# Performance work log

Measured on AMD Instinct MI355X. Metric: run time of the kernel, lower is better.

Reference implementation:

```python
import jax, jax.numpy as jnp
import numpy as np

B, N, C_IN, C_OUT = 16, 1024, 256, 256
POOL_RATIO = 0.5  # pooling_ration


def setup_inputs() -> dict:
    key = jax.random.key(0)
    k0, k1, k2, k3 = jax.random.split(key, 4)
    x = jax.random.normal(k0, (B, N, C_IN), dtype=jnp.float32)
    # sparse-ish dense adjacency (as the module stores adj densely)
    adj = (jax.random.uniform(k1, (B, N, N)) < 0.02).astype(jnp.float32)
    mask = jnp.ones((B, N), dtype=jnp.int32)
    n_nodes = jnp.full((B,), N, dtype=jnp.int32)
    stdv = 1.0 / np.sqrt(C_IN)
    W = jax.random.uniform(k2, (C_IN, C_OUT), minval=-stdv, maxval=stdv, dtype=jnp.float32)
    b = jnp.zeros((C_OUT,), dtype=jnp.float32)
    pooling = jax.random.uniform(k3, (C_OUT, 1), minval=-1.0, maxval=1.0, dtype=jnp.float32)
    return {"x": x, "adj": adj, "mask": mask, "n_nodes": n_nodes, "W": W, "b": b, "pooling": pooling}


def reference(x, adj, mask, n_nodes, W, b, pooling):
    # GraphConvolutionLayer: adj @ (x W) + b   (standard Kipf GCN layer)
    h = jnp.einsum('bnm,bmc->bnc', adj, x @ W) + b          # [B,N,C_OUT]
    Bm, Nm, C = h.shape
    # projection score y = (h @ pooling) / ||pooling||
    y = (h.reshape(Bm * Nm, C) @ pooling).reshape(Bm, Nm)
    y = y / jnp.sqrt(jnp.sum(pooling ** 2))
    # ascending sort indices
    idx = jnp.argsort(y, axis=1)                            # [B,N]
    n_remove = (n_nodes.astype(jnp.float32) * (1.0 - POOL_RATIO)).astype(jnp.int32)
    new_n_nodes = n_nodes - n_remove
    # vectorized equivalent of the per-batch loop: among currently-masked nodes
    # (in ascending-score order), zero out the first n_remove[b] of them.
    m_sorted = jnp.take_along_axis(mask, idx, axis=1)       # mask gathered in sorted order
    rank = jnp.cumsum(m_sorted, axis=1) - m_sorted          # exclusive rank among masked
    remove = (m_sorted == 1) & (rank < n_remove[:, None])
    new_sorted = jnp.where(remove, 0, m_sorted)
    inv = jnp.argsort(idx, axis=1)                          # inverse permutation
    new_mask = jnp.take_along_axis(new_sorted, inv, axis=1)  # [B,N] int
    mf = new_mask.astype(h.dtype)
    x_out = h * jnp.tanh(y)[:, :, None] * mf[:, :, None]
    adj_out = mf[:, :, None] * adj * mf[:, None, :]
    return x_out, adj_out, new_mask, new_n_nodes
```

## Files before the change

kernel.cpp:

```cpp
#include <hip/hip_runtime.h>
#include <math.h>

#define Bsz 16
#define Nn  1024

#define ADJ_OFF    (16*1024*256)
#define MASK_OFF   (ADJ_OFF + 16*1024*1024)
#define NN_OFF     (MASK_OFF + 16*1024)

typedef unsigned long long u64;
typedef unsigned short u16;
typedef short bf16x8 __attribute__((ext_vector_type(8)));
typedef float f32x4  __attribute__((ext_vector_type(4)));

static __device__ inline u16 f2bf(float f) {
    unsigned u = __float_as_uint(f);
    u += 0x7fffu + ((u >> 16) & 1u);
    return (u16)(u >> 16);
}

__global__ __launch_bounds__(256) void k1(const float* __restrict__ x,
                                          const float* __restrict__ W,
                                          const float* __restrict__ pool,
                                          u16* __restrict__ XB,
                                          u16* __restrict__ WT,
                                          float* __restrict__ Z) {
    int bid = blockIdx.x, t = threadIdx.x, lane = t & 63, wid = t >> 6;
    if (bid < 256) {
        __shared__ float sp[256];
        __shared__ float swp[256];
        sp[t] = pool[t];
        __syncthreads();
        float acc = 0.f;
        const float* wr = W + t * 256;
        for (int j = 0; j < 256; j += 4) {
            float4 w4 = *(const float4*)&wr[j];
            acc = fmaf(w4.x, sp[j], fmaf(w4.y, sp[j + 1],
                  fmaf(w4.z, sp[j + 2], fmaf(w4.w, sp[j + 3], acc))));
        }
        swp[t] = acc;
        __syncthreads();
        const float* w4p = &swp[lane * 4];
        float wx = w4p[0], wy = w4p[1], wz = w4p[2], ww = w4p[3];
        int base = bid * 64 + wid * 16;
        #pragma unroll 1
        for (int rb = 0; rb < 4; ++rb) {
            float4 v[4];
            #pragma unroll
            for (int k = 0; k < 4; ++k)
                v[k] = ((const float4*)(x + (size_t)(base + rb * 4 + k) * 256))[lane];
            #pragma unroll
            for (int k = 0; k < 4; ++k) {
                int row = base + rb * 4 + k;
                ushort4 o;
                o.x = f2bf(v[k].x); o.y = f2bf(v[k].y); o.z = f2bf(v[k].z); o.w = f2bf(v[k].w);
                ((ushort4*)(XB + (size_t)row * 256))[lane] = o;
                float a = fmaf(v[k].x, wx, fmaf(v[k].y, wy, fmaf(v[k].z, wz, v[k].w * ww)));
                for (int off = 32; off > 0; off >>= 1) a += __shfl_down(a, off, 64);
                if (lane == 0) Z[row] = a;
            }
        }
    } else {
        __shared__ float sT[64][65];
        int bt = bid - 256;
        int tr = (bt >> 2) * 64, tc = (bt & 3) * 64;
        #pragma unroll
        for (int p = 0; p < 4; ++p) {
            int r = p * 16 + (t >> 4), c = (t & 15) * 4;
            float4 w = *(const float4*)&W[(size_t)(tr + r) * 256 + tc + c];
            sT[r][c] = w.x; sT[r][c + 1] = w.y; sT[r][c + 2] = w.z; sT[r][c + 3] = w.w;
        }
        __syncthreads();
        #pragma unroll
        for (int p = 0; p < 2; ++p) {
            int nl = p * 32 + (t >> 3), kl = (t & 7) * 8;
            u16 tmp[8];
            #pragma unroll
            for (int j = 0; j < 8; ++j) tmp[j] = f2bf(sT[kl + j][nl]);
            *(int4*)&WT[(size_t)(tc + nl) * 256 + tr + kl] = *(const int4*)tmp;
        }
    }
}

__global__ __launch_bounds__(256) void k2(const u16* __restrict__ XB,
                                          const u16* __restrict__ WT,
                                          const float* __restrict__ adj,
                                          const float* __restrict__ Z,
                                          u16* __restrict__ XWBT,
                                          u16* __restrict__ AB,
                                          float* __restrict__ Y) {
    int t = threadIdx.x, lane = t & 63, wid = t >> 6;
    if (blockIdx.x < 256) {
        __shared__ short sA[128][72];
        __shared__ short sB[128][72];
        int bm = blockIdx.x >> 1, bn = blockIdx.x & 1;
        int wave = wid;
        int wr = (wave >> 1) * 64, wc = (wave & 1) * 64;
        int fm = lane & 15, fq = lane >> 4;

        f32x4 acc[4][4];
        #pragma unroll
        for (int i = 0; i < 4; ++i)
            #pragma unroll
            for (int j = 0; j < 4; ++j)
                acc[i][j] = (f32x4){0.f, 0.f, 0.f, 0.f};

        int sr = t >> 1, half = (t & 1) * 32;
        const u16* gA = XB + ((size_t)(bm * 128 + sr)) * 256 + half;
        const u16* gB = WT + ((size_t)(bn * 128 + sr)) * 256 + half;

        for (int kt = 0; kt < 4; ++kt) {
            __syncthreads();
            #pragma unroll
            for (int q = 0; q < 4; ++q) {
                *(int4*)&sA[sr][half + q * 8] = *(const int4*)&gA[kt * 64 + q * 8];
                *(int4*)&sB[sr][half + q * 8] = *(const int4*)&gB[kt * 64 + q * 8];
            }
            __syncthreads();
            #pragma unroll
            for (int ks = 0; ks < 64; ks += 32) {
                bf16x8 af[4], bfv[4];
                #pragma unroll
                for (int i = 0; i < 4; ++i)
                    af[i] = *(const bf16x8*)&sA[wr + i * 16 + fm][ks + fq * 8];
                #pragma unroll
                for (int j = 0; j < 4; ++j)
                    bfv[j] = *(const bf16x8*)&sB[wc + j * 16 + fm][ks + fq * 8];
                #pragma unroll
                for (int i = 0; i < 4; ++i)
                    #pragma unroll
                    for (int j = 0; j < 4; ++j)
                        acc[i][j] = __builtin_amdgcn_mfma_f32_16x16x32_bf16(af[i], bfv[j], acc[i][j], 0, 0, 0);
            }
        }
        int b = bm >> 3;
        #pragma unroll
        for (int i = 0; i < 4; ++i) {
            int rloc = (bm & 7) * 128 + wr + i * 16 + fq * 4;
            #pragma unroll
            for (int j = 0; j < 4; ++j) {
                int c = bn * 128 + wc + j * 16 + fm;
                u16 tmp[4];
                #pragma unroll
                for (int r = 0; r < 4; ++r) tmp[r] = f2bf(acc[i][j][r]);
                *(unsigned long long*)&XWBT[(size_t)b * 262144 + (size_t)c * 1024 + rloc] =
                    *(const unsigned long long*)tmp;
            }
        }
    } else {
        int g = blockIdx.x - 256;
        int b = g >> 6, grp = g & 63;
        __shared__ float sZ[1024];
        ((float4*)sZ)[t] = ((const float4*)(Z + (b << 10)))[t];
        __syncthreads();
        const float* z0 = &sZ[lane * 4];
        #pragma unroll 1
        for (int rr = 0; rr < 4; ++rr) {
            int row = (b << 10) + grp * 16 + wid * 4 + rr;
            const float4* ar = (const float4*)(adj + (size_t)row * 1024);
            float4 v0 = ar[lane], v1 = ar[64 + lane], v2 = ar[128 + lane], v3 = ar[192 + lane];
            u16* abr = AB + (size_t)row * 1024;
            ushort4 o0, o1, o2, o3;
            o0.x = f2bf(v0.x); o0.y = f2bf(v0.y); o0.z = f2bf(v0.z); o0.w = f2bf(v0.w);
            o1.x = f2bf(v1.x); o1.y = f2bf(v1.y); o1.z = f2bf(v1.z); o1.w = f2bf(v1.w);
            o2.x = f2bf(v2.x); o2.y = f2bf(v2.y); o2.z = f2bf(v2.z); o2.w = f2bf(v2.w);
            o3.x = f2bf(v3.x); o3.y = f2bf(v3.y); o3.z = f2bf(v3.z); o3.w = f2bf(v3.w);
            ((ushort4*)abr)[lane] = o0;
            ((ushort4*)abr)[64 + lane] = o1;
            ((ushort4*)abr)[128 + lane] = o2;
            ((ushort4*)abr)[192 + lane] = o3;
            float a = v0.x * z0[0] + v0.y * z0[1] + v0.z * z0[2] + v0.w * z0[3];
            a += v1.x * z0[256] + v1.y * z0[257] + v1.z * z0[258] + v1.w * z0[259];
            a += v2.x * z0[512] + v2.y * z0[513] + v2.z * z0[514] + v2.w * z0[515];
            a += v3.x * z0[768] + v3.y * z0[769] + v3.z * z0[770] + v3.w * z0[771];
            for (int off = 32; off > 0; off >>= 1) a += __shfl_down(a, off, 64);
            if (lane == 0) Y[row] = a;
        }
    }
}

__device__ inline u64 shfl_xor_u64(u64 v, int m) {
    int lo = __shfl_xor((int)(v & 0xffffffffULL), m, 64);
    int hi = __shfl_xor((int)(v >> 32), m, 64);
    return ((u64)(unsigned)hi << 32) | (unsigned)lo;
}

__global__ __launch_bounds__(1024) void k3(const float* __restrict__ Y,
                                           const int* __restrict__ maskIn,
                                           const int* __restrict__ nNodes,
                                           const float* __restrict__ bias,
                                           const float* __restrict__ pool,
                                           float* __restrict__ SCALE,
                                           float* __restrict__ NM,
                                           float* __restrict__ newN,
                                           u64* __restrict__ NMBITS) {
    __shared__ u64 s[1024];
    __shared__ int wsum[16];
    __shared__ int nmLoc[1024];
    __shared__ float redb[4], redq[4];
    __shared__ float sBP, sINV;

    int b = blockIdx.x, t = threadIdx.x, lane = t & 63, wid = t >> 6;
    int base = b << 10;

    if (t < 256) {
        float pv = pool[t];
        float bv = bias[t] * pv;
        float qv = pv * pv;
        for (int off = 32; off > 0; off >>= 1) {
            bv += __shfl_down(bv, off, 64);
            qv += __shfl_down(qv, off, 64);
        }
        if (lane == 0) { redb[wid] = bv; redq[wid] = qv; }
    }
    __syncthreads();
    if (t == 0) {
        sBP  = redb[0] + redb[1] + redb[2] + redb[3];
        sINV = 1.0f / sqrtf(redq[0] + redq[1] + redq[2] + redq[3]);
    }

    float ky = Y[base + t];
    unsigned u = __float_as_uint(ky);
    u = (u & 0x80000000u) ? ~u : (u | 0x80000000u);
    u64 val = ((u64)u << 32) | (unsigned)t;

    for (int k = 2; k <= 1024; k <<= 1) {
        bool up = ((t & k) == 0);
        int j = k >> 1;
        for (; j >= 64; j >>= 1) {
            s[t] = val; __syncthreads();
            u64 p = s[t ^ j]; __syncthreads();
            bool keepMin = (up == ((t & j) == 0));
            bool pLess = p < val;
            val = (keepMin == pLess) ? p : val;
        }
        for (; j >= 1; j >>= 1) {
            u64 p = shfl_xor_u64(val, j);
            bool keepMin = (up == ((t & j) == 0));
            bool pLess = p < val;
            val = (keepMin == pLess) ? p : val;
        }
    }

    int idx = (int)(val & 1023u);
    int mval = maskIn[base + idx];
    int sc = mval;
    for (int off = 1; off < 64; off <<= 1) {
        int nv = __shfl_up(sc, off, 64);
        if (lane >= off) sc += nv;
    }
    if (lane == 63) wsum[wid] = sc;
    __syncthreads();
    int offset = 0;
    for (int w = 0; w < wid; ++w) offset += wsum[w];
    int rank = sc + offset - mval;
    int nn = nNodes[b];
    int nrem = (int)((float)nn * 0.5f);
    int nm = (mval == 1 && rank < nrem) ? 0 : mval;
    nmLoc[idx] = nm;
    NM[base + idx] = (float)nm;
    if (t == 0) newN[b] = (float)(nn - nrem);
    __syncthreads();

    int myNm = nmLoc[t];
    u64 bmask = __ballot(myNm != 0);
    if (lane == 0) NMBITS[b * 16 + wid] = bmask;
    float yr = Y[base + t];
    SCALE[base + t] = myNm ? tanhf((yr + sBP) * sINV) : 0.0f;
}

__global__ __launch_bounds__(256) void k4(const u16* __restrict__ AB,
                                          const u16* __restrict__ XWBT,
                                          const float* __restrict__ SCALE,
                                          const float* __restrict__ bias,
                                          const u64* __restrict__ NMBITS,
                                          float* __restrict__ XO,
                                          float* __restrict__ AO) {
    int t = threadIdx.x, lane = t & 63, wid = t >> 6;
    if (blockIdx.x < 256) {
        __shared__ short sA[128][72];
        __shared__ short sB[128][72];
        int idx = blockIdx.x;
        int bn = idx & 1, bmt = (idx >> 1) & 7, b = idx >> 4;
        int wr = (wid >> 1) * 64, wc = (wid & 1) * 64;
        int fm = lane & 15, fq = lane >> 4;

        f32x4 acc[4][4];
        #pragma unroll
        for (int i = 0; i < 4; ++i)
            #pragma unroll
            for (int j = 0; j < 4; ++j)
                acc[i][j] = (f32x4){0.f, 0.f, 0.f, 0.f};

        int sr = t >> 1, half = (t & 1) * 32;
        const u16* gA = AB + ((size_t)(b * 1024 + bmt * 128 + sr)) * 1024 + half;
        const u16* gB = XWBT + (size_t)b * 262144 + (size_t)(bn * 128 + sr) * 1024 + half;

        for (int kt = 0; kt < 16; ++kt) {
            __syncthreads();
            #pragma unroll
            for (int q = 0; q < 4; ++q) {
                *(int4*)&sA[sr][half + q * 8] = *(const int4*)&gA[kt * 64 + q * 8];
                *(int4*)&sB[sr][half + q * 8] = *(const int4*)&gB[kt * 64 + q * 8];
            }
            __syncthreads();
            #pragma unroll
            for (int ks = 0; ks < 64; ks += 32) {
                bf16x8 af[4], bfv[4];
                #pragma unroll
                for (int i = 0; i < 4; ++i)
                    af[i] = *(const bf16x8*)&sA[wr + i * 16 + fm][ks + fq * 8];
                #pragma unroll
                for (int j = 0; j < 4; ++j)
                    bfv[j] = *(const bf16x8*)&sB[wc + j * 16 + fm][ks + fq * 8];
                #pragma unroll
                for (int i = 0; i < 4; ++i)
                    #pragma unroll
                    for (int j = 0; j < 4; ++j)
                        acc[i][j] = __builtin_amdgcn_mfma_f32_16x16x32_bf16(af[i], bfv[j], acc[i][j], 0, 0, 0);
            }
        }
        float bj[4];
        #pragma unroll
        for (int j = 0; j < 4; ++j) bj[j] = bias[bn * 128 + wc + j * 16 + fm];
        int mb = (b << 10) + bmt * 128 + wr;
        #pragma unroll
        for (int i = 0; i < 4; ++i) {
            int m0 = mb + i * 16 + fq * 4;
            float s0 = SCALE[m0], s1 = SCALE[m0 + 1], s2 = SCALE[m0 + 2], s3 = SCALE[m0 + 3];
            #pragma unroll
            for (int j = 0; j < 4; ++j) {
                int c = bn * 128 + wc + j * 16 + fm;
                float* xo = XO + (size_t)m0 * 256 + c;
                xo[0]   = (acc[i][j][0] + bj[j]) * s0;
                xo[256] = (acc[i][j][1] + bj[j]) * s1;
                xo[512] = (acc[i][j][2] + bj[j]) * s2;
                xo[768] = (acc[i][j][3] + bj[j]) * s3;
            }
        }
    } else {
        int g = blockIdx.x - 256;
        int b = g >> 6, grp = g & 63;
        __shared__ u64 sBits[16];
        if (t < 16) sBits[t] = NMBITS[b * 16 + t];
        __syncthreads();
        int c0 = t * 4;
        u64 wb = sBits[c0 >> 6] >> (c0 & 63);
        float m0 = (wb & 1) ? 1.f : 0.f;
        float m1 = ((wb >> 1) & 1) ? 1.f : 0.f;
        float m2 = ((wb >> 2) & 1) ? 1.f : 0.f;
        float m3 = ((wb >> 3) & 1) ? 1.f : 0.f;
        #pragma unroll 1
        for (int r = 0; r < 16; ++r) {
            int rloc = grp * 16 + r;
            int nmRow = (int)((sBits[rloc >> 6] >> (rloc & 63)) & 1ULL);
            float4* aor = (float4*)(AO + (size_t)((b << 10) + rloc) * 1024);
            if (nmRow) {
                ushort4 ab = ((const ushort4*)(AB + (size_t)((b << 10) + rloc) * 1024))[t];
                float4 o;
                o.x = ab.x ? m0 : 0.f;
                o.y = ab.y ? m1 : 0.f;
                o.z = ab.z ? m2 : 0.f;
                o.w = ab.w ? m3 : 0.f;
                aor[t] = o;
            } else {
                aor[t] = make_float4(0.f, 0.f, 0.f, 0.f);
            }
        }
    }
}

extern "C" void kernel_launch(void* const* d_in, const int* in_sizes, int n_in,
                              void* d_out, int out_size, void* d_ws, size_t ws_size,
                              hipStream_t stream) {
    const float* x      = (const float*)d_in[0];
    const float* adj    = (const float*)d_in[1];
    const int*   mask   = (const int*)d_in[2];
    const int*   nnodes = (const int*)d_in[3];
    const float* W      = (const float*)d_in[4];
    const float* bias   = (const float*)d_in[5];
    const float* pool   = (const float*)d_in[6];

    float* out = (float*)d_out;
    float* XO  = out;
    float* AO  = out + ADJ_OFF;
    float* NM  = out + MASK_OFF;
    float* NNo = out + NN_OFF;

    char* w = (char*)d_ws;
    u16*   XB     = (u16*)(w);
    u16*   WT     = (u16*)(w + 8388608);
    u16*   XWBT   = (u16*)(w + 8519680);
    u16*   AB     = (u16*)(w + 16908288);
    float* Z      = (float*)(w + 50462720);
    float* Y      = (float*)(w + 50528256);
    float* SCALE  = (float*)(w + 50593792);
    u64*   NMBITS = (u64*)(w + 50659328);

    k1<<<272, 256, 0, stream>>>(x, W, pool, XB, WT, Z);
    k2<<<1280, 256, 0, stream>>>(XB, WT, adj, Z, XWBT, AB, Y);
    k3<<<Bsz, 1024, 0, stream>>>(Y, mask, nnodes, bias, pool, SCALE, NM, NNo, NMBITS);
    k4<<<1280, 256, 0, stream>>>(AB, XWBT, SCALE, bias, NMBITS, XO, AO);
}
```

Before: 207.0 us.

## Fuse adjacency masking into GEMM, drop bf16 adj buffer, rank-count sort

k2 no longer writes a bf16 copy of the adjacency. k4 now reads fp32 adj directly, converts it to bf16 into shared memory for the MFMA GEMM and writes the masked adj_out from the same load. This removes a full write and re-read of a 32MB intermediate. k3 replaces the single-block-per-batch bitonic sort with a per-element O(N) rank count spread over 4 blocks per batch. The cost is more shared-memory comparison work in k3 and a smaller GEMM tile (32x256) in k4, which reloads the B operand 32 times per batch.

```diff
diff --git a/kernel.cpp b/kernel.cpp
--- a/kernel.cpp
+++ b/kernel.cpp
@@ -87,15 +87,13 @@
                                           const float* __restrict__ adj,
                                           const float* __restrict__ Z,
                                           u16* __restrict__ XWBT,
-                                          u16* __restrict__ AB,
                                           float* __restrict__ Y) {
     int t = threadIdx.x, lane = t & 63, wid = t >> 6;
     if (blockIdx.x < 256) {
         __shared__ short sA[128][72];
         __shared__ short sB[128][72];
         int bm = blockIdx.x >> 1, bn = blockIdx.x & 1;
-        int wave = wid;
-        int wr = (wave >> 1) * 64, wc = (wave & 1) * 64;
+        int wr = (wid >> 1) * 64, wc = (wid & 1) * 64;
         int fm = lane & 15, fq = lane >> 4;
 
         f32x4 acc[4][4];
@@ -159,16 +157,6 @@
             int row = (b << 10) + grp * 16 + wid * 4 + rr;
             const float4* ar = (const float4*)(adj + (size_t)row * 1024);
             float4 v0 = ar[lane], v1 = ar[64 + lane], v2 = ar[128 + lane], v3 = ar[192 + lane];
-            u16* abr = AB + (size_t)row * 1024;
-            ushort4 o0, o1, o2, o3;
-            o0.x = f2bf(v0.x); o0.y = f2bf(v0.y); o0.z = f2bf(v0.z); o0.w = f2bf(v0.w);
-            o1.x = f2bf(v1.x); o1.y = f2bf(v1.y); o1.z = f2bf(v1.z); o1.w = f2bf(v1.w);
-            o2.x = f2bf(v2.x); o2.y = f2bf(v2.y); o2.z = f2bf(v2.z); o2.w = f2bf(v2.w);
-            o3.x = f2bf(v3.x); o3.y = f2bf(v3.y); o3.z = f2bf(v3.z); o3.w = f2bf(v3.w);
-            ((ushort4*)abr)[lane] = o0;
-            ((ushort4*)abr)[64 + lane] = o1;
-            ((ushort4*)abr)[128 + lane] = o2;
-            ((ushort4*)abr)[192 + lane] = o3;
             float a = v0.x * z0[0] + v0.y * z0[1] + v0.z * z0[2] + v0.w * z0[3];
             a += v1.x * z0[256] + v1.y * z0[257] + v1.z * z0[258] + v1.w * z0[259];
             a += v2.x * z0[512] + v2.y * z0[513] + v2.z * z0[514] + v2.w * z0[515];
@@ -179,31 +167,28 @@
     }
 }
 
-__device__ inline u64 shfl_xor_u64(u64 v, int m) {
-    int lo = __shfl_xor((int)(v & 0xffffffffULL), m, 64);
-    int hi = __shfl_xor((int)(v >> 32), m, 64);
-    return ((u64)(unsigned)hi << 32) | (unsigned)lo;
-}
-
-__global__ __launch_bounds__(1024) void k3(const float* __restrict__ Y,
-                                           const int* __restrict__ maskIn,
-                                           const int* __restrict__ nNodes,
-                                           const float* __restrict__ bias,
-                                           const float* __restrict__ pool,
-                                           float* __restrict__ SCALE,
-                                           float* __restrict__ NM,
-                                           float* __restrict__ newN,
-                                           u64* __restrict__ NMBITS) {
-    __shared__ u64 s[1024];
-    __shared__ int wsum[16];
-    __shared__ int nmLoc[1024];
+__global__ __launch_bounds__(256) void k3(const float* __restrict__ Y,
+                                          const int* __restrict__ maskIn,
+                                          const int* __restrict__ nNodes,
+                                          const float* __restrict__ bias,
+                                          const float* __restrict__ pool,
+                                          float* __restrict__ SCALE,
+                                          float* __restrict__ NM,
+                                          float* __restrict__ newN,
+                                          u64* __restrict__ NMBITS) {
+    __shared__ float sy[1024];
+    __shared__ int   sm[1024];
     __shared__ float redb[4], redq[4];
     __shared__ float sBP, sINV;
-
-    int b = blockIdx.x, t = threadIdx.x, lane = t & 63, wid = t >> 6;
+    int b = blockIdx.x >> 2, part = blockIdx.x & 3;
+    int t = threadIdx.x, lane = t & 63, wid = t >> 6;
     int base = b << 10;
 
-    if (t < 256) {
+    for (int j = t; j < 1024; j += 256) {
+        sy[j] = Y[base + j];
+        sm[j] = maskIn[base + j];
+    }
+    {
         float pv = pool[t];
         float bv = bias[t] * pv;
         float qv = pv * pv;
@@ -218,154 +203,127 @@
         sBP  = redb[0] + redb[1] + redb[2] + redb[3];
         sINV = 1.0f / sqrtf(redq[0] + redq[1] + redq[2] + redq[3]);
     }
-
-    float ky = Y[base + t];
-    unsigned u = __float_as_uint(ky);
-    u = (u & 0x80000000u) ? ~u : (u | 0x80000000u);
-    u64 val = ((u64)u << 32) | (unsigned)t;
-
-    for (int k = 2; k <= 1024; k <<= 1) {
-        bool up = ((t & k) == 0);
-        int j = k >> 1;
-        for (; j >= 64; j >>= 1) {
-            s[t] = val; __syncthreads();
-            u64 p = s[t ^ j]; __syncthreads();
-            bool keepMin = (up == ((t & j) == 0));
-            bool pLess = p < val;
-            val = (keepMin == pLess) ? p : val;
-        }
-        for (; j >= 1; j >>= 1) {
-            u64 p = shfl_xor_u64(val, j);
-            bool keepMin = (up == ((t & j) == 0));
-            bool pLess = p < val;
-            val = (keepMin == pLess) ? p : val;
-        }
-    }
-
-    int idx = (int)(val & 1023u);
-    int mval = maskIn[base + idx];
-    int sc = mval;
-    for (int off = 1; off < 64; off <<= 1) {
-        int nv = __shfl_up(sc, off, 64);
-        if (lane >= off) sc += nv;
-    }
-    if (lane == 63) wsum[wid] = sc;
     __syncthreads();
-    int offset = 0;
-    for (int w = 0; w < wid; ++w) offset += wsum[w];
-    int rank = sc + offset - mval;
+
+    int i = part * 256 + t;
+    float yi = sy[i];
+    int cnt = 0;
+    #pragma unroll 4
+    for (int j = 0; j < 1024; ++j) {
+        float yj = sy[j];
+        bool less = (yj < yi) || (yj == yi && j < i);
+        cnt += less ? sm[j] : 0;
+    }
     int nn = nNodes[b];
     int nrem = (int)((float)nn * 0.5f);
-    int nm = (mval == 1 && rank < nrem) ? 0 : mval;
-    nmLoc[idx] = nm;
-    NM[base + idx] = (float)nm;
-    if (t == 0) newN[b] = (float)(nn - nrem);
-    __syncthreads();
-
-    int myNm = nmLoc[t];
-    u64 bmask = __ballot(myNm != 0);
-    if (lane == 0) NMBITS[b * 16 + wid] = bmask;
-    float yr = Y[base + t];
-    SCALE[base + t] = myNm ? tanhf((yr + sBP) * sINV) : 0.0f;
-}
-
-__global__ __launch_bounds__(256) void k4(const u16* __restrict__ AB,
+    int mi = sm[i];
+    int nm = (mi == 1 && cnt < nrem) ? 0 : mi;
+    NM[base + i] = (float)nm;
+    SCALE[base + i] = nm ? tanhf((yi + sBP) * sINV) : 0.0f;
+    u64 bm = __ballot(nm != 0);
+    if (lane == 0) NMBITS[b * 16 + part * 4 + wid] = bm;
+    if (t == 0 && part == 0) newN[b] = (float)(nn - nrem);
+}
+
+__global__ __launch_bounds__(256) void k4(const float* __restrict__ adj,
                                           const u16* __restrict__ XWBT,
                                           const float* __restrict__ SCALE,
                                           const float* __restrict__ bias,
                                           const u64* __restrict__ NMBITS,
                                           float* __restrict__ XO,
                                           float* __restrict__ AO) {
+    __shared__ short sA[32][72];
+    __shared__ short sB[256][72];
+    __shared__ u64 sBits[16];
     int t = threadIdx.x, lane = t & 63, wid = t >> 6;
-    if (blockIdx.x < 256) {
-        __shared__ short sA[128][72];
-        __shared__ short sB[128][72];
-        int idx = blockIdx.x;
-        int bn = idx & 1, bmt = (idx >> 1) & 7, b = idx >> 4;
-        int wr = (wid >> 1) * 64, wc = (wid & 1) * 64;
-        int fm = lane & 15, fq = lane >> 4;
-
-        f32x4 acc[4][4];
-        #pragma unroll
-        for (int i = 0; i < 4; ++i)
+    int b = blockIdx.x >> 5, mt = blockIdx.x & 31;
+    int m0 = mt * 32;
+    if (t < 16) sBits[t] = NMBITS[b * 16 + t];
+
+    int wc = wid * 64;
+    int fm = lane & 15, fq = lane >> 4;
+
+    f32x4 acc[2][4];
+    #pragma unroll
+    for (int i = 0; i < 2; ++i)
+        #pragma unroll
+        for (int j = 0; j < 4; ++j)
+            acc[i][j] = (f32x4){0.f, 0.f, 0.f, 0.f};
+
+    int ar = t >> 3, c8 = (t & 7) * 8;
+    const float* adjR = adj + ((size_t)((b << 10) + m0 + ar)) * 1024 + c8;
+    float*       aoR  = AO  + ((size_t)((b << 10) + m0 + ar)) * 1024 + c8;
+    const u16*   xwB  = XWBT + (size_t)b * 262144;
+
+    __syncthreads();
+    int rloc = m0 + ar;
+    float rowM = (float)((sBits[rloc >> 6] >> (rloc & 63)) & 1ULL);
+
+    for (int kt = 0; kt < 16; ++kt) {
+        int k0 = kt * 64;
+        __syncthreads();
+        {
+            float4 v0 = *(const float4*)&adjR[k0];
+            float4 v1 = *(const float4*)&adjR[k0 + 4];
+            unsigned cb = (unsigned)((sBits[(k0 + c8) >> 6] >> ((k0 + c8) & 63)) & 0xffULL);
+            float4 o0, o1;
+            o0.x = (cb & 1u)   ? v0.x * rowM : 0.f;
+            o0.y = (cb & 2u)   ? v0.y * rowM : 0.f;
+            o0.z = (cb & 4u)   ? v0.z * rowM : 0.f;
+            o0.w = (cb & 8u)   ? v0.w * rowM : 0.f;
+            o1.x = (cb & 16u)  ? v1.x * rowM : 0.f;
+            o1.y = (cb & 32u)  ? v1.y * rowM : 0.f;
+            o1.z = (cb & 64u)  ? v1.z * rowM : 0.f;
+            o1.w = (cb & 128u) ? v1.w * rowM : 0.f;
+            *(float4*)&aoR[k0] = o0;
+            *(float4*)&aoR[k0 + 4] = o1;
+            u16 tmp[8];
+            tmp[0] = f2bf(v0.x); tmp[1] = f2bf(v0.y); tmp[2] = f2bf(v0.z); tmp[3] = f2bf(v0.w);
+            tmp[4] = f2bf(v1.x); tmp[5] = f2bf(v1.y); tmp[6] = f2bf(v1.z); tmp[7] = f2bf(v1.w);
+            *(int4*)&sA[ar][c8] = *(const int4*)tmp;
+        }
+        {
+            int nb = t >> 3;
+            #pragma unroll
+            for (int pass = 0; pass < 8; ++pass) {
+                int n = nb + pass * 32;
+                *(int4*)&sB[n][c8] = *(const int4*)&xwB[(size_t)n * 1024 + k0 + c8];
+            }
+        }
+        __syncthreads();
+        #pragma unroll
+        for (int ks = 0; ks < 64; ks += 32) {
+            bf16x8 af[2], bfv[4];
+            #pragma unroll
+            for (int i = 0; i < 2; ++i)
+                af[i] = *(const bf16x8*)&sA[i * 16 + fm][ks + fq * 8];
             #pragma unroll
             for (int j = 0; j < 4; ++j)
-                acc[i][j] = (f32x4){0.f, 0.f, 0.f, 0.f};
-
-        int sr = t >> 1, half = (t & 1) * 32;
-        const u16* gA = AB + ((size_t)(b * 1024 + bmt * 128 + sr)) * 1024 + half;
-        const u16* gB = XWBT + (size_t)b * 262144 + (size_t)(bn * 128 + sr) * 1024 + half;
-
-        for (int kt = 0; kt < 16; ++kt) {
-            __syncthreads();
-            #pragma unroll
-            for (int q = 0; q < 4; ++q) {
-                *(int4*)&sA[sr][half + q * 8] = *(const int4*)&gA[kt * 64 + q * 8];
-                *(int4*)&sB[sr][half + q * 8] = *(const int4*)&gB[kt * 64 + q * 8];
-            }
-            __syncthreads();
-            #pragma unroll
-            for (int ks = 0; ks < 64; ks += 32) {
-                bf16x8 af[4], bfv[4];
-                #pragma unroll
-                for (int i = 0; i < 4; ++i)
-                    af[i] = *(const bf16x8*)&sA[wr + i * 16 + fm][ks + fq * 8];
+                bfv[j] = *(const bf16x8*)&sB[wc + j * 16 + fm][ks + fq * 8];
+            #pragma unroll
+            for (int i = 0; i < 2; ++i)
                 #pragma unroll
                 for (int j = 0; j < 4; ++j)
-                    bfv[j] = *(const bf16x8*)&sB[wc + j * 16 + fm][ks + fq * 8];
-                #pragma unroll
-                for (int i = 0; i < 4; ++i)
-                    #pragma unroll
-                    for (int j = 0; j < 4; ++j)
-                        acc[i][j] = __builtin_amdgcn_mfma_f32_16x16x32_bf16(af[i], bfv[j], acc[i][j], 0, 0, 0);
-            }
-        }
-        float bj[4];
-        #pragma unroll
-        for (int j = 0; j < 4; ++j) bj[j] = bias[bn * 128 + wc + j * 16 + fm];
-        int mb = (b << 10) + bmt * 128 + wr;
-        #pragma unroll
-        for (int i = 0; i < 4; ++i) {
-            int m0 = mb + i * 16 + fq * 4;
-            float s0 = SCALE[m0], s1 = SCALE[m0 + 1], s2 = SCALE[m0 + 2], s3 = SCALE[m0 + 3];
-            #pragma unroll
-            for (int j = 0; j < 4; ++j) {
-                int c = bn * 128 + wc + j * 16 + fm;
-                float* xo = XO + (size_t)m0 * 256 + c;
-                xo[0]   = (acc[i][j][0] + bj[j]) * s0;
-                xo[256] = (acc[i][j][1] + bj[j]) * s1;
-                xo[512] = (acc[i][j][2] + bj[j]) * s2;
-                xo[768] = (acc[i][j][3] + bj[j]) * s3;
-            }
-        }
-    } else {
-        int g = blockIdx.x - 256;
-        int b = g >> 6, grp = g & 63;
-        __shared__ u64 sBits[16];
-        if (t < 16) sBits[t] = NMBITS[b * 16 + t];
-        __syncthreads();
-        int c0 = t * 4;
-        u64 wb = sBits[c0 >> 6] >> (c0 & 63);
-        float m0 = (wb & 1) ? 1.f : 0.f;
-        float m1 = ((wb >> 1) & 1) ? 1.f : 0.f;
-        float m2 = ((wb >> 2) & 1) ? 1.f : 0.f;
-        float m3 = ((wb >> 3) & 1) ? 1.f : 0.f;
-        #pragma unroll 1
-        for (int r = 0; r < 16; ++r) {
-            int rloc = grp * 16 + r;
-            int nmRow = (int)((sBits[rloc >> 6] >> (rloc & 63)) & 1ULL);
-            float4* aor = (float4*)(AO + (size_t)((b << 10) + rloc) * 1024);
-            if (nmRow) {
-                ushort4 ab = ((const ushort4*)(AB + (size_t)((b << 10) + rloc) * 1024))[t];
-                float4 o;
-                o.x = ab.x ? m0 : 0.f;
-                o.y = ab.y ? m1 : 0.f;
-                o.z = ab.z ? m2 : 0.f;
-                o.w = ab.w ? m3 : 0.f;
-                aor[t] = o;
-            } else {
-                aor[t] = make_float4(0.f, 0.f, 0.f, 0.f);
-            }
+                    acc[i][j] = __builtin_amdgcn_mfma_f32_16x16x32_bf16(af[i], bfv[j], acc[i][j], 0, 0, 0);
+        }
+    }
+
+    float bj[4];
+    #pragma unroll
+    for (int j = 0; j < 4; ++j) bj[j] = bias[wc + j * 16 + fm];
+    int mb = (b << 10) + m0;
+    #pragma unroll
+    for (int i = 0; i < 2; ++i) {
+        int r0 = mb + i * 16 + fq * 4;
+        float s0 = SCALE[r0], s1 = SCALE[r0 + 1], s2 = SCALE[r0 + 2], s3 = SCALE[r0 + 3];
+        #pragma unroll
+        for (int j = 0; j < 4; ++j) {
+            int c = wc + j * 16 + fm;
+            float* xo = XO + (size_t)r0 * 256 + c;
+            xo[0]   = (acc[i][j][0] + bj[j]) * s0;
+            xo[256] = (acc[i][j][1] + bj[j]) * s1;
+            xo[512] = (acc[i][j][2] + bj[j]) * s2;
+            xo[768] = (acc[i][j][3] + bj[j]) * s3;
         }
     }
 }
@@ -391,14 +349,13 @@
     u16*   XB     = (u16*)(w);
     u16*   WT     = (u16*)(w + 8388608);
     u16*   XWBT   = (u16*)(w + 8519680);
-    u16*   AB     = (u16*)(w + 16908288);
-    float* Z      = (float*)(w + 50462720);
-    float* Y      = (float*)(w + 50528256);
-    float* SCALE  = (float*)(w + 50593792);
-    u64*   NMBITS = (u64*)(w + 50659328);
+    float* Z      = (float*)(w + 16908288);
+    float* Y      = (float*)(w + 16973824);
+    float* SCALE  = (float*)(w + 17039360);
+    u64*   NMBITS = (u64*)(w + 17104896);
 
     k1<<<272, 256, 0, stream>>>(x, W, pool, XB, WT, Z);
-    k2<<<1280, 256, 0, stream>>>(XB, WT, adj, Z, XWBT, AB, Y);
-    k3<<<Bsz, 1024, 0, stream>>>(Y, mask, nnodes, bias, pool, SCALE, NM, NNo, NMBITS);
-    k4<<<1280, 256, 0, stream>>>(AB, XWBT, SCALE, bias, NMBITS, XO, AO);
-}
+    k2<<<1280, 256, 0, stream>>>(XB, WT, adj, Z, XWBT, Y);
+    k3<<<Bsz * 4, 256, 0, stream>>>(Y, mask, nnodes, bias, pool, SCALE, NM, NNo, NMBITS);
+    k4<<<512, 256, 0, stream>>>(adj, XWBT, SCALE, bias, NMBITS, XO, AO);
+}
```

New measurement: 226.3 us. +9.3%, slower.

## Replace bitonic sort in k3 with per-node rank counting across 64 blocks

Applied to the files above, without the earlier changes.

The per-batch bitonic sort plus prefix scan in k3 is replaced by direct rank counting: each node counts the masked nodes with a smaller score (ties broken by index), which gives its exclusive masked rank without building a permutation. The work is split across 4 blocks of 256 threads per batch instead of one 1024-thread block, so more CUs are used and the many block-wide barriers of the sort go away. In exchange each thread does O(N) shared-memory reads, about a million comparisons per batch, and every block reloads the full Y and mask rows.

```diff
diff --git a/kernel.cpp b/kernel.cpp
--- a/kernel.cpp
+++ b/kernel.cpp
@@ -94,8 +94,7 @@
         __shared__ short sA[128][72];
         __shared__ short sB[128][72];
         int bm = blockIdx.x >> 1, bn = blockIdx.x & 1;
-        int wave = wid;
-        int wr = (wave >> 1) * 64, wc = (wave & 1) * 64;
+        int wr = (wid >> 1) * 64, wc = (wid & 1) * 64;
         int fm = lane & 15, fq = lane >> 4;
 
         f32x4 acc[4][4];
@@ -179,31 +178,28 @@
     }
 }
 
-__device__ inline u64 shfl_xor_u64(u64 v, int m) {
-    int lo = __shfl_xor((int)(v & 0xffffffffULL), m, 64);
-    int hi = __shfl_xor((int)(v >> 32), m, 64);
-    return ((u64)(unsigned)hi << 32) | (unsigned)lo;
-}
-
-__global__ __launch_bounds__(1024) void k3(const float* __restrict__ Y,
-                                           const int* __restrict__ maskIn,
-                                           const int* __restrict__ nNodes,
-                                           const float* __restrict__ bias,
-                                           const float* __restrict__ pool,
-                                           float* __restrict__ SCALE,
-                                           float* __restrict__ NM,
-                                           float* __restrict__ newN,
-                                           u64* __restrict__ NMBITS) {
-    __shared__ u64 s[1024];
-    __shared__ int wsum[16];
-    __shared__ int nmLoc[1024];
+__global__ __launch_bounds__(256) void k3(const float* __restrict__ Y,
+                                          const int* __restrict__ maskIn,
+                                          const int* __restrict__ nNodes,
+                                          const float* __restrict__ bias,
+                                          const float* __restrict__ pool,
+                                          float* __restrict__ SCALE,
+                                          float* __restrict__ NM,
+                                          float* __restrict__ newN,
+                                          u64* __restrict__ NMBITS) {
+    __shared__ float sy[1024];
+    __shared__ int   sm[1024];
     __shared__ float redb[4], redq[4];
     __shared__ float sBP, sINV;
-
-    int b = blockIdx.x, t = threadIdx.x, lane = t & 63, wid = t >> 6;
+    int b = blockIdx.x >> 2, part = blockIdx.x & 3;
+    int t = threadIdx.x, lane = t & 63, wid = t >> 6;
     int base = b << 10;
 
-    if (t < 256) {
+    for (int j = t; j < 1024; j += 256) {
+        sy[j] = Y[base + j];
+        sm[j] = maskIn[base + j];
+    }
+    {
         float pv = pool[t];
         float bv = bias[t] * pv;
         float qv = pv * pv;
@@ -218,55 +214,26 @@
         sBP  = redb[0] + redb[1] + redb[2] + redb[3];
         sINV = 1.0f / sqrtf(redq[0] + redq[1] + redq[2] + redq[3]);
     }
-
-    float ky = Y[base + t];
-    unsigned u = __float_as_uint(ky);
-    u = (u & 0x80000000u) ? ~u : (u | 0x80000000u);
-    u64 val = ((u64)u << 32) | (unsigned)t;
-
-    for (int k = 2; k <= 1024; k <<= 1) {
-        bool up = ((t & k) == 0);
-        int j = k >> 1;
-        for (; j >= 64; j >>= 1) {
-            s[t] = val; __syncthreads();
-            u64 p = s[t ^ j]; __syncthreads();
-            bool keepMin = (up == ((t & j) == 0));
-            bool pLess = p < val;
-            val = (keepMin == pLess) ? p : val;
-        }
-        for (; j >= 1; j >>= 1) {
-            u64 p = shfl_xor_u64(val, j);
-            bool keepMin = (up == ((t & j) == 0));
-            bool pLess = p < val;
-            val = (keepMin == pLess) ? p : val;
-        }
-    }
-
-    int idx = (int)(val & 1023u);
-    int mval = maskIn[base + idx];
-    int sc = mval;
-    for (int off = 1; off < 64; off <<= 1) {
-        int nv = __shfl_up(sc, off, 64);
-        if (lane >= off) sc += nv;
-    }
-    if (lane == 63) wsum[wid] = sc;
     __syncthreads();
-    int offset = 0;
-    for (int w = 0; w < wid; ++w) offset += wsum[w];
-    int rank = sc + offset - mval;
+
+    int i = part * 256 + t;
+    float yi = sy[i];
+    int cnt = 0;
+    #pragma unroll 4
+    for (int j = 0; j < 1024; ++j) {
+        float yj = sy[j];
+        bool less = (yj < yi) || (yj == yi && j < i);
+        cnt += less ? sm[j] : 0;
+    }
     int nn = nNodes[b];
     int nrem = (int)((float)nn * 0.5f);
-    int nm = (mval == 1 && rank < nrem) ? 0 : mval;
-    nmLoc[idx] = nm;
-    NM[base + idx] = (float)nm;
-    if (t == 0) newN[b] = (float)(nn - nrem);
-    __syncthreads();
-
-    int myNm = nmLoc[t];
-    u64 bmask = __ballot(myNm != 0);
-    if (lane == 0) NMBITS[b * 16 + wid] = bmask;
-    float yr = Y[base + t];
-    SCALE[base + t] = myNm ? tanhf((yr + sBP) * sINV) : 0.0f;
+    int mi = sm[i];
+    int nm = (mi == 1 && cnt < nrem) ? 0 : mi;
+    NM[base + i] = (float)nm;
+    SCALE[base + i] = nm ? tanhf((yi + sBP) * sINV) : 0.0f;
+    u64 bm = __ballot(nm != 0);
+    if (lane == 0) NMBITS[b * 16 + part * 4 + wid] = bm;
+    if (t == 0 && part == 0) newN[b] = (float)(nn - nrem);
 }
 
 __global__ __launch_bounds__(256) void k4(const u16* __restrict__ AB,
@@ -399,6 +366,6 @@
 
     k1<<<272, 256, 0, stream>>>(x, W, pool, XB, WT, Z);
     k2<<<1280, 256, 0, stream>>>(XB, WT, adj, Z, XWBT, AB, Y);
-    k3<<<Bsz, 1024, 0, stream>>>(Y, mask, nnodes, bias, pool, SCALE, NM, NNo, NMBITS);
+    k3<<<Bsz * 4, 256, 0, stream>>>(Y, mask, nnodes, bias, pool, SCALE, NM, NNo, NMBITS);
     k4<<<1280, 256, 0, stream>>>(AB, XWBT, SCALE, bias, NMBITS, XO, AO);
 }
```

After: 228.5 us. +10.4%, slower.
